# Performance work log

Measured on AMD Instinct MI355X. Metric: run time of the kernel, lower is better.

The kernel has to match this reference:

```python
import jax, jax.numpy as jnp
import numpy as np
from jax import lax

B, C, L, K = 8, 256, 4096, 65
PAD = K // 2  # torch: int(kernel.shape[-1] / 2) = 32 -> same-length output for odd K


def depthwise_corr(x, k):
    """Depthwise cross-correlation (torch conv1d semantics, no kernel flip).
    x: [B, C, L] float32, k: [K] float32 (same kernel shared by all channels,
    matching kernel.repeat(seq_len, 1)). Returns [B, C, L]."""
    w = jnp.broadcast_to(k.reshape(1, 1, K), (C, 1, K))  # [C, 1, K]
    return lax.conv_general_dilated(
        x, w, window_strides=(1,), padding=[(PAD, PAD)],
        dimension_numbers=("NCH", "OIH", "NCH"), feature_group_count=C)


def setup_inputs() -> dict:
    key = jax.random.key(0)
    k1, k2, k3 = jax.random.split(key, 3)
    return {
        "x": jax.random.normal(k1, (B, C, L), dtype=jnp.float32),
        "kernel_real": jax.random.normal(k2, (K,), dtype=jnp.float32),
        "kernel_imag": jax.random.normal(k3, (K,), dtype=jnp.float32),
        "weights_mag": jnp.ones((1, C, 1), dtype=jnp.float32),
        "weights_angle": jnp.ones((1, C, 1), dtype=jnp.float32),
    }


def reference(x, kernel_real, kernel_imag, weights_mag, weights_angle):
    # mf_coeffs = conj(kernel) -> weight = kernel_real - 1j*kernel_imag.
    # Input x is real (imag=0 after .to(complex64)), so complex conv splits
    # into two real depthwise correlations.
    yr = depthwise_corr(x, kernel_real)            # [B, C, L]
    yi = -depthwise_corr(x, kernel_imag)           # [B, C, L]
    y = lax.complex(yr, yi)                        # complex64 [B, C, L]

    # torch.std over dims (1,2), unbiased (correction=1), complex -> real std
    mean = jnp.mean(y, axis=(1, 2), keepdims=True)
    n = C * L
    var = jnp.sum(jnp.abs(y - mean) ** 2, axis=(1, 2), keepdims=True) / (n - 1)
    y = y / jnp.sqrt(var)                          # real std broadcasts over complex

    # weights_mag * y * exp(-1j * weights_angle)
    phase = lax.complex(jnp.cos(weights_angle), -jnp.sin(weights_angle))  # [1, C, 1]
    y = weights_mag * y * phase

    # FFT over the channel dim (dim=-2), then fftshift on that dim
    return jnp.fft.fftshift(jnp.fft.fft(y, axis=-2), axes=-2)
```

## Files before the change

### kernel.cpp

```cpp
#include <hip/hip_runtime.h>
#include <math.h>

#define NB 8
#define NC 256
#define NL 4096
#define NK 65
#define NSL (NL / 16)

__device__ float4 g_part[NB * NSL];

__device__ __forceinline__ int lidx(int row, int q) {
    return (row << 3) + (q ^ (row & 7));
}

#define LOAD16(W, off)                                                      \
    {                                                                       \
        const int g0_ = l0 + (off);                                         \
        if (g0_ >= 0 && g0_ + 16 <= NL) {         \
            _Pragma("unroll")                                               \
            for (int q = 0; q < 4; ++q) {                                   \
                const float4 v_ = *(const float4*)(xr + g0_ + 4 * q);       \
                W[4*q+0] = v_.x; W[4*q+1] = v_.y;                           \
                W[4*q+2] = v_.z; W[4*q+3] = v_.w;                           \
            }                                                               \
        } else {                                                            \
            _Pragma("unroll")                                               \
            for (int q = 0; q < 16; ++q) {                                  \
                const int g_ = g0_ + q;                                     \
                W[q] = (g_ >= 0 && g_ < NL) ? xr[g_] : 0.0f;                \
            }                                                               \
        }                                                                   \
    }

#define CHUNK16(Lo, Hi, tb)                                                 \
    {                                                                       \
        _Pragma("unroll")                                                   \
        for (int j2 = 0; j2 < 16; ++j2) {                                   \
            const float kr_ = kre[(tb) + j2];        \
            const float ki_ = kim[(tb) + j2];                               \
            _Pragma("unroll")                                               \
            for (int i = 0; i < 16; ++i) {                                  \
                const int wi_ = i + j2;                                     \
                const float xv_ = (wi_ < 16) ? Lo[wi_] : Hi[wi_ - 16];      \
                sr[i] = fmaf(xv_, kr_, sr[i]);                              \
                si[i] = fmaf(xv_, ki_, si[i]);                              \
            }                                                               \
        }                                                                   \
    }

__device__ __forceinline__ int digitrev_shift(int pp) {
    int k = ((pp & 3) << 6) | (((pp >> 2) & 3) << 4)
          | (((pp >> 4) & 3) << 2) | ((pp >> 6) & 3);
    return k ^ 128;
}

__global__ __launch_bounds__(256, 5) void fused_conv_fft_kernel(
    const float* __restrict__ x,
    const float* __restrict__ kre,
    const float* __restrict__ kim,
    const float* __restrict__ wmag,
    const float* __restrict__ wang,
    float* __restrict__ out,
    int out_size)
{
    __shared__ __align__(16) float4 lbuf4[NC * 8];

    const int t = threadIdx.x;
    const int b = blockIdx.x & 7;
    const int st = blockIdx.x >> 3;
    const int l0 = st << 4;
    const int lane = t & 63, wv = t >> 6;

    float tw64r, tw64i;
    {
        float ang = (float)lane * 0.024543692606170260f;
        float s, c;
        sincosf(ang, &s, &c);
        tw64r = c; tw64i = -s;
    }
    float sw, cw;
    sincosf(wang[t], &sw, &cw);
    const float wm = wmag[t];
    const float wgr =  wm * cw;
    const float wgi = -wm * sw;

    const float* xr = x + (size_t)b * NC * NL + (size_t)t * NL;
    const bool interleaved = (out_size >= 2 * NB * NC * NL);

    float sr[16], si[16];
    #pragma unroll
    for (int i = 0; i < 16; ++i) { sr[i] = 0.0f; si[i] = 0.0f; }

    float A[16], B[16];
    LOAD16(A, -32);
    LOAD16(B, -16);
    CHUNK16(A, B, 0);
    LOAD16(A, 0);
    CHUNK16(B, A, 16);
    LOAD16(B, 16);
    CHUNK16(A, B, 32);
    LOAD16(A, 32);
    CHUNK16(B, A, 48);
    {
        const float kr_ = kre[64];
        const float ki_ = kim[64];
        #pragma unroll
        for (int i = 0; i < 16; ++i) {
            sr[i] = fmaf(A[i], kr_, sr[i]);
            si[i] = fmaf(A[i], ki_, si[i]);
        }
    }

    float tsr = 0.0f, tsi = 0.0f, tsq = 0.0f;
    #pragma unroll
    for (int i = 0; i < 16; ++i) {
        tsr += sr[i];
        tsi -= si[i];
        tsq = fmaf(sr[i], sr[i], tsq);
        tsq = fmaf(si[i], si[i], tsq);
    }

    #pragma unroll
    for (int k = 0; k < 8; ++k) {
        float4 o;
        o.x = sr[2*k]   * wgr + si[2*k]   * wgi;
        o.y = sr[2*k]   * wgi - si[2*k]   * wgr;
        o.z = sr[2*k+1] * wgr + si[2*k+1] * wgi;
        o.w = sr[2*k+1] * wgi - si[2*k+1] * wgr;
        lbuf4[lidx(t, k)] = o;
    }
    __syncthreads();

    #pragma unroll
    for (int s = 0; s < 4; ++s) {
        const int shift = 2 * s;
        const int q = 64 >> shift;
        #pragma unroll
        for (int it = 0; it < 2; ++it) {
            int task = it * 256 + t;
            int lpp = task & 7;
            int m = task >> 3;
            int j = m & (q - 1);
            int blk = m >> (6 - shift);
            int base2 = blk << (8 - shift);

            int ca = base2 + j;
            float4 a0 = lbuf4[lidx(ca, lpp)];
            float4 a1 = lbuf4[lidx(ca + q, lpp)];
            float4 a2 = lbuf4[lidx(ca + 2*q, lpp)];
            float4 a3 = lbuf4[lidx(ca + 3*q, lpp)];

            float w1r, w1i;
            if (s < 3) {
                int e = j << shift;
                w1r = __shfl(tw64r, e);
                w1i = __shfl(tw64i, e);
            } else {
                w1r = 1.0f; w1i = 0.0f;
            }
            float w2r = fmaf(w1r, w1r, -(w1i * w1i));
            float w2i = 2.0f * w1r * w1i;
            float w3r = w2r * w1r - w2i * w1i;
            float w3i = w2r * w1i + w2i * w1r;

            float4 b0, b1, b2, b3;
            {
                float t0r = a0.x + a2.x, t0i = a0.y + a2.y;
                float t1r = a0.x - a2.x, t1i = a0.y - a2.y;
                float t2r = a1.x + a3.x, t2i = a1.y + a3.y;
                float t3r = a1.x - a3.x, t3i = a1.y - a3.y;
                b0.x = t0r + t2r;       b0.y = t0i + t2i;
                float b2r = t0r - t2r,  b2i = t0i - t2i;
                float b1r = t1r + t3i,  b1i = t1i - t3r;
                float b3r = t1r - t3i,  b3i = t1i + t3r;
                b1.x = b1r*w1r - b1i*w1i;  b1.y = b1r*w1i + b1i*w1r;
                b2.x = b2r*w2r - b2i*w2i;  b2.y = b2r*w2i + b2i*w2r;
                b3.x = b3r*w3r - b3i*w3i;  b3.y = b3r*w3i + b3i*w3r;
            }
            {
                float t0r = a0.z + a2.z, t0i = a0.w + a2.w;
                float t1r = a0.z - a2.z, t1i = a0.w - a2.w;
                float t2r = a1.z + a3.z, t2i = a1.w + a3.w;
                float t3r = a1.z - a3.z, t3i = a1.w - a3.w;
                b0.z = t0r + t2r;       b0.w = t0i + t2i;
                float b2r = t0r - t2r,  b2i = t0i - t2i;
                float b1r = t1r + t3i,  b1i = t1i - t3r;
                float b3r = t1r - t3i,  b3i = t1i + t3r;
                b1.z = b1r*w1r - b1i*w1i;  b1.w = b1r*w1i + b1i*w1r;
                b2.z = b2r*w2r - b2i*w2i;  b2.w = b2r*w2i + b2i*w2r;
                b3.z = b3r*w3r - b3i*w3i;  b3.w = b3r*w3i + b3i*w3r;
            }
            lbuf4[lidx(ca, lpp)]         = b0;
            lbuf4[lidx(ca + q, lpp)]     = b1;
            lbuf4[lidx(ca + 2*q, lpp)]   = b2;
            lbuf4[lidx(ca + 3*q, lpp)]   = b3;
        }
        __syncthreads();
    }

    #pragma unroll
    for (int it = 0; it < 8; ++it) {
        int task = it * 256 + t;
        int lpp = task & 7;
        int pp = task >> 3;
        float4 v = lbuf4[lidx(pp, lpp)];
        int cout = digitrev_shift(pp);
        if (interleaved) {
            size_t fi = 2 * ((size_t)(b * NC + cout) * NL + l0) + 4 * lpp;
            if (fi + 4 <= (size_t)out_size) *(float4*)(out + fi) = v;
        } else {
            size_t fi = (size_t)(b * NC + cout) * NL + l0 + 2 * lpp;
            if (fi + 2 <= (size_t)out_size) {
                float2 o2; o2.x = v.x; o2.y = v.z;
                *(float2*)(out + fi) = o2;
            }
        }
    }

    #pragma unroll
    for (int off = 32; off > 0; off >>= 1) {
        tsr += __shfl_down(tsr, off);
        tsi += __shfl_down(tsi, off);
        tsq += __shfl_down(tsq, off);
    }
    __syncthreads();
    float* redf = (float*)lbuf4;
    if (lane == 0) { redf[wv*3+0] = tsr; redf[wv*3+1] = tsi; redf[wv*3+2] = tsq; }
    __syncthreads();
    if (t == 0) {
        float a0 = 0.0f, a1 = 0.0f, a2 = 0.0f;
        #pragma unroll
        for (int i = 0; i < 4; ++i) { a0 += redf[i*3]; a1 += redf[i*3+1]; a2 += redf[i*3+2]; }
        g_part[b * NSL + st] = make_float4(a0, a1, a2, 0.0f);
    }
}

__global__ __launch_bounds__(256) void scale_out_kernel(
    float* __restrict__ out, int out_size)
{
    __shared__ float sred[13];
    const int t = threadIdx.x;
    const int j = blockIdx.x;
    const int b = j >> 8;
    const int lane = t & 63, wv = t >> 6;

    float4 p = g_part[b * NSL + t];
    float psr = p.x, psi = p.y, psq = p.z;
    #pragma unroll
    for (int off = 32; off > 0; off >>= 1) {
        psr += __shfl_down(psr, off);
        psi += __shfl_down(psi, off);
        psq += __shfl_down(psq, off);
    }
    if (lane == 0) { sred[wv*3+0] = psr; sred[wv*3+1] = psi; sred[wv*3+2] = psq; }
    __syncthreads();
    if (t == 0) {
        float a0 = 0.0f, a1 = 0.0f, a2 = 0.0f;
        #pragma unroll
        for (int i = 0; i < 4; ++i) { a0 += sred[i*3]; a1 += sred[i*3+1]; a2 += sred[i*3+2]; }
        const float n = (float)(NC * NL);
        float var = (a2 - (a0*a0 + a1*a1)/n) / (n - 1.0f);
        sred[12] = rsqrtf(var);
    }
    __syncthreads();
    const float inv = sred[12];

    const int fpb = out_size >> 11;
    const int base = j * fpb;
    if ((fpb & 3) == 0 && ((size_t)(out + base) & 15) == 0) {
        float4* o4 = (float4*)(out + base);
        const int n4 = fpb >> 2;
        for (int i = t; i < n4; i += 256) {
            float4 v = o4[i];
            v.x *= inv; v.y *= inv; v.z *= inv; v.w *= inv;
            o4[i] = v;
        }
    } else {
        for (int i = t; i < fpb; i += 256) out[base + i] *= inv;
    }
    if (j == 2047) {
        for (int i = (fpb << 11) + t; i < out_size; i += 256) out[i] *= inv;
    }
}

extern "C" void kernel_launch(void* const* d_in, const int* in_sizes, int n_in,
                              void* d_out, int out_size, void* d_ws, size_t ws_size,
                              hipStream_t stream)
{
    const float* x   = (const float*)d_in[0];
    const float* kre = (const float*)d_in[1];
    const float* kim = (const float*)d_in[2];
    const float* wm  = (const float*)d_in[3];
    const float* wa  = (const float*)d_in[4];
    float* out = (float*)d_out;
    (void)d_ws; (void)ws_size;

    fused_conv_fft_kernel<<<NB * NSL, 256, 0, stream>>>(x, kre, kim, wm, wa,
                                                        out, out_size);
    scale_out_kernel<<<2048, 256, 0, stream>>>(out, out_size);
}
```

Before: 147.1 us.

## Preload all conv windows, use nontemporal stores, interleave scale blocks across batches

The conv stage now issues all four input window loads before the FMA chunks so more global-load latency overlaps compute, and the sincos setup is moved after the convolution. Output writes in both kernels use nontemporal stores/loads, and the scale kernel maps blocks so consecutive blocks touch different batches. Occupancy hint drops from 5 to 4 waves per SIMD to allow the extra registers, and LDS grows slightly. The tail handling in the scale kernel is mostly preserved but the segment arithmetic changed, which risks subtle coverage gaps for unusual out_size values.

```diff
diff --git a/kernel.cpp b/kernel.cpp
--- a/kernel.cpp
+++ b/kernel.cpp
@@ -6,6 +6,9 @@
 #define NL 4096
 #define NK 65
 #define NSL (NL / 16)
+
+typedef float vf4 __attribute__((ext_vector_type(4)));
+typedef float vf2 __attribute__((ext_vector_type(2)));
 
 __device__ float4 g_part[NB * NSL];
 
@@ -54,7 +57,7 @@
     return k ^ 128;
 }
 
-__global__ __launch_bounds__(256, 5) void fused_conv_fft_kernel(
+__global__ __launch_bounds__(256, 4) void fused_conv_fft_kernel(
     const float* __restrict__ x,
     const float* __restrict__ kre,
     const float* __restrict__ kim,
@@ -63,7 +66,7 @@
     float* __restrict__ out,
     int out_size)
 {
-    __shared__ __align__(16) float4 lbuf4[NC * 8];
+    __shared__ __align__(16) float4 lbuf4[NC * 9];
 
     const int t = threadIdx.x;
     const int b = blockIdx.x & 7;
@@ -71,53 +74,53 @@
     const int l0 = st << 4;
     const int lane = t & 63, wv = t >> 6;
 
+    const float* xr = x + (size_t)b * NC * NL + (size_t)t * NL;
+    const bool interleaved = (out_size >= 2 * NB * NC * NL);
+
+    float sr[16], si[16];
+    #pragma unroll
+    for (int i = 0; i < 16; ++i) { sr[i] = 0.0f; si[i] = 0.0f; }
+
+    float W0[16], W1[16], W2[16], W3[16];
+    LOAD16(W0, -32);
+    LOAD16(W1, -16);
+    LOAD16(W2, 0);
+    LOAD16(W3, 16);
+    CHUNK16(W0, W1, 0);
+    LOAD16(W0, 32);
+    CHUNK16(W1, W2, 16);
+    CHUNK16(W2, W3, 32);
+    CHUNK16(W3, W0, 48);
+    {
+        const float kr_ = kre[64];
+        const float ki_ = kim[64];
+        #pragma unroll
+        for (int i = 0; i < 16; ++i) {
+            sr[i] = fmaf(W0[i], kr_, sr[i]);
+            si[i] = fmaf(W0[i], ki_, si[i]);
+        }
+    }
+
+    float tsr = 0.0f, tsi = 0.0f, tsq = 0.0f;
+    #pragma unroll
+    for (int i = 0; i < 16; ++i) {
+        tsr += sr[i];
+        tsi -= si[i];
+        tsq = fmaf(sr[i], sr[i], tsq);
+        tsq = fmaf(si[i], si[i], tsq);
+    }
+
+    float sw, cw;
+    sincosf(wang[t], &sw, &cw);
+    const float wm = wmag[t];
+    const float wgr =  wm * cw;
+    const float wgi = -wm * sw;
     float tw64r, tw64i;
     {
         float ang = (float)lane * 0.024543692606170260f;
         float s, c;
         sincosf(ang, &s, &c);
         tw64r = c; tw64i = -s;
-    }
-    float sw, cw;
-    sincosf(wang[t], &sw, &cw);
-    const float wm = wmag[t];
-    const float wgr =  wm * cw;
-    const float wgi = -wm * sw;
-
-    const float* xr = x + (size_t)b * NC * NL + (size_t)t * NL;
-    const bool interleaved = (out_size >= 2 * NB * NC * NL);
-
-    float sr[16], si[16];
-    #pragma unroll
-    for (int i = 0; i < 16; ++i) { sr[i] = 0.0f; si[i] = 0.0f; }
-
-    float A[16], B[16];
-    LOAD16(A, -32);
-    LOAD16(B, -16);
-    CHUNK16(A, B, 0);
-    LOAD16(A, 0);
-    CHUNK16(B, A, 16);
-    LOAD16(B, 16);
-    CHUNK16(A, B, 32);
-    LOAD16(A, 32);
-    CHUNK16(B, A, 48);
-    {
-        const float kr_ = kre[64];
-        const float ki_ = kim[64];
-        #pragma unroll
-        for (int i = 0; i < 16; ++i) {
-            sr[i] = fmaf(A[i], kr_, sr[i]);
-            si[i] = fmaf(A[i], ki_, si[i]);
-        }
-    }
-
-    float tsr = 0.0f, tsi = 0.0f, tsq = 0.0f;
-    #pragma unroll
-    for (int i = 0; i < 16; ++i) {
-        tsr += sr[i];
-        tsi -= si[i];
-        tsq = fmaf(sr[i], sr[i], tsq);
-        tsq = fmaf(si[i], si[i], tsq);
     }
 
     #pragma unroll
@@ -207,12 +210,15 @@
         int cout = digitrev_shift(pp);
         if (interleaved) {
             size_t fi = 2 * ((size_t)(b * NC + cout) * NL + l0) + 4 * lpp;
-            if (fi + 4 <= (size_t)out_size) *(float4*)(out + fi) = v;
+            if (fi + 4 <= (size_t)out_size) {
+                vf4 o4; o4.x = v.x; o4.y = v.y; o4.z = v.z; o4.w = v.w;
+                __builtin_nontemporal_store(o4, (vf4*)(out + fi));
+            }
         } else {
             size_t fi = (size_t)(b * NC + cout) * NL + l0 + 2 * lpp;
             if (fi + 2 <= (size_t)out_size) {
-                float2 o2; o2.x = v.x; o2.y = v.z;
-                *(float2*)(out + fi) = o2;
+                vf2 o2; o2.x = v.x; o2.y = v.z;
+                __builtin_nontemporal_store(o2, (vf2*)(out + fi));
             }
         }
     }
@@ -241,7 +247,8 @@
     __shared__ float sred[13];
     const int t = threadIdx.x;
     const int j = blockIdx.x;
-    const int b = j >> 8;
+    const int b = j & 7;
+    const int seg = j >> 3;
     const int lane = t & 63, wv = t >> 6;
 
     float4 p = g_part[b * NSL + t];
@@ -265,21 +272,23 @@
     __syncthreads();
     const float inv = sred[12];
 
-    const int fpb = out_size >> 11;
-    const int base = j * fpb;
-    if ((fpb & 3) == 0 && ((size_t)(out + base) & 15) == 0) {
-        float4* o4 = (float4*)(out + base);
-        const int n4 = fpb >> 2;
+    const int fpbatch = out_size >> 3;
+    const int fpseg = fpbatch >> 8;
+    const int base = b * fpbatch + seg * fpseg;
+    if ((fpseg & 3) == 0 && ((size_t)(out + base) & 15) == 0) {
+        const int n4 = fpseg >> 2;
         for (int i = t; i < n4; i += 256) {
-            float4 v = o4[i];
+            vf4* p4 = (vf4*)(out + base) + i;
+            vf4 v = __builtin_nontemporal_load(p4);
             v.x *= inv; v.y *= inv; v.z *= inv; v.w *= inv;
-            o4[i] = v;
+            __builtin_nontemporal_store(v, p4);
         }
     } else {
-        for (int i = t; i < fpb; i += 256) out[base + i] *= inv;
+        for (int i = t; i < fpseg; i += 256) out[base + i] *= inv;
     }
     if (j == 2047) {
-        for (int i = (fpb << 11) + t; i < out_size; i += 256) out[i] *= inv;
+        for (int i = ((out_size >> 11) << 11) + t; i < out_size; i += 256)
+            out[i] *= inv;
     }
 }
 
```

New measurement: 141.7 us. -3.7%, faster.
